# Kernel tuning notes

Hardware: AMD Instinct MI355X
Metric: run time of the kernel (lower is better)

The kernel has to match this reference:

```python
import jax, jax.numpy as jnp
import numpy as np

ALPHA = 1.0
BETA = 0.5

B, N, E = 4096, 4096, 16384


def setup_inputs() -> dict:
    key = jax.random.key(0)
    k1, k2, k3, k4, k5 = jax.random.split(key, 5)
    outputs = jax.random.normal(k1, (B, N), dtype=jnp.float32)
    targets = jax.random.uniform(k2, (B, N), dtype=jnp.float32)
    # per-node level weight (equivalent to node_levels dict -> level_weights lookup)
    level_w = jax.random.uniform(k3, (N,), dtype=jnp.float32)
    edge_src = jax.random.randint(k4, (E,), 0, N, dtype=jnp.int32)  # parent i
    edge_dst = jax.random.randint(k5, (E,), 0, N, dtype=jnp.int32)  # child  j
    return {"outputs": outputs, "targets": targets, "level_w": level_w,
            "edge_src": edge_src, "edge_dst": edge_dst}


def reference(outputs, targets, level_w, edge_src, edge_dst):
    # BCEWithLogits, reduction='none': softplus(x) - x*t (numerically stable)
    bce = jax.nn.softplus(outputs) - outputs * targets          # [B, N]
    weighted_bce = bce * level_w[None, :]                        # [B, N]

    probs = jax.nn.sigmoid(outputs)                              # [B, N]
    # for each edge (i=parent, j=child): consistency[:, j] += relu(p[:, j] - p[:, i])
    diff = jax.nn.relu(probs[:, edge_dst] - probs[:, edge_src])  # [B, E]
    consistency = jnp.zeros_like(probs).at[:, edge_dst].add(diff)  # [B, N]

    return ALPHA * weighted_bce.mean() + BETA * consistency.mean()
```

## Files before the change

### kernel.cpp

```cpp
#include <hip/hip_runtime.h>
#include <math.h>


#define ALPHA_C 1.0f
#define BETA_C  0.5f

constexpr int B = 4096;
constexpr int N = 4096;
constexpr int E = 16384;
constexpr int THREADS = 1024;
constexpr int R = 4;
constexpr int GRID = 256;
constexpr int GPB = (B / R) / GRID;
constexpr int EJ = E / 4 / THREADS;

typedef _Float16 h4 __attribute__((ext_vector_type(4)));

__global__ __launch_bounds__(64) void init_out_kernel(float* out) {
    if (threadIdx.x == 0) out[0] = 0.0f;
}

__device__ __forceinline__ void fast_sig_sp(float x, float& p, float& sp) {
    float q = __expf(-fabsf(x));
    float d = 1.0f + q;
    float r = __builtin_amdgcn_rcpf(d);
    p  = (x >= 0.0f) ? r : q * r;
    sp = fmaxf(x, 0.0f) + __logf(d);
}

__global__ __launch_bounds__(THREADS, 4) void hier_loss_kernel(
    const float* __restrict__ outputs,
    const float* __restrict__ targets,
    const float* __restrict__ level_w,
    const int*   __restrict__ edge_src,
    const int*   __restrict__ edge_dst,
    float*       __restrict__ out)
{
    __shared__ h4 P[2][N];

    const int tid = threadIdx.x;
    const int g0  = blockIdx.x * GPB;

    const float4* out4 = (const float4*)outputs;
    const float4* tgt4 = (const float4*)targets;
    const float4* lw4  = (const float4*)level_w;
    const int4*   es4  = (const int4*)edge_src;
    const int4*   ed4  = (const int4*)edge_dst;

    const float4 w = lw4[tid];
    const float wv[4] = {w.x, w.y, w.z, w.w};

    int4 se[EJ], de[EJ];
#pragma unroll
    for (int j = 0; j < EJ; ++j) {
        se[j] = es4[tid + j * THREADS];
        de[j] = ed4[tid + j * THREADS];
    }

    float s1 = 0.0f, s2 = 0.0f;
    float4 xs[R], ts[R];

#pragma unroll
    for (int r = 0; r < R; ++r) {
        const size_t row = (size_t)((g0 + 0) * R + r) * (N / 4) + tid;
        xs[r] = out4[row];
        ts[r] = tgt4[row];
    }
    {
        h4 tmp[4];
#pragma unroll
        for (int r = 0; r < R; ++r) {
            const float xv[4] = {xs[r].x, xs[r].y, xs[r].z, xs[r].w};
            const float tv[4] = {ts[r].x, ts[r].y, ts[r].z, ts[r].w};
#pragma unroll
            for (int k = 0; k < 4; ++k) {
                float p, sp;
                fast_sig_sp(xv[k], p, sp);
                s1 = fmaf(wv[k], sp - xv[k] * tv[k], s1);
                tmp[k][r] = (_Float16)p;
            }
        }
#pragma unroll
        for (int k = 0; k < 4; ++k) P[0][4 * tid + k] = tmp[k];
    }
    __syncthreads();

#pragma unroll
    for (int kg = 0; kg < GPB; ++kg) {
        if (kg + 1 < GPB) {
#pragma unroll
            for (int r = 0; r < R; ++r) {
                const size_t row = (size_t)((g0 + kg + 1) * R + r) * (N / 4) + tid;
                xs[r] = out4[row];
                ts[r] = tgt4[row];
            }
        }

        const h4* Pc = P[kg & 1];
        h4 acc0 = {0, 0, 0, 0};
        h4 acc1 = {0, 0, 0, 0};
        const h4 zero = {0, 0, 0, 0};
#pragma unroll
        for (int j = 0; j < EJ; ++j) {
            const int4 s = se[j];
            const int4 d = de[j];
            h4 a0 = Pc[s.x], c0 = Pc[d.x];
            h4 a1 = Pc[s.y], c1 = Pc[d.y];
            h4 a2 = Pc[s.z], c2 = Pc[d.z];
            h4 a3 = Pc[s.w], c3 = Pc[d.w];
            acc0 += __builtin_elementwise_max(c0 - a0, zero);
            acc1 += __builtin_elementwise_max(c1 - a1, zero);
            acc0 += __builtin_elementwise_max(c2 - a2, zero);
            acc1 += __builtin_elementwise_max(c3 - a3, zero);
        }
#pragma unroll
        for (int l = 0; l < 4; ++l) s2 += (float)acc0[l] + (float)acc1[l];

        if (kg + 1 < GPB) {
            h4 tmp[4];
#pragma unroll
            for (int r = 0; r < R; ++r) {
                const float xv[4] = {xs[r].x, xs[r].y, xs[r].z, xs[r].w};
                const float tv[4] = {ts[r].x, ts[r].y, ts[r].z, ts[r].w};
#pragma unroll
                for (int k = 0; k < 4; ++k) {
                    float p, sp;
                    fast_sig_sp(xv[k], p, sp);
                    s1 = fmaf(wv[k], sp - xv[k] * tv[k], s1);
                    tmp[k][r] = (_Float16)p;
                }
            }
#pragma unroll
            for (int k = 0; k < 4; ++k) P[(kg + 1) & 1][4 * tid + k] = tmp[k];
        }
        __syncthreads();
    }

#pragma unroll
    for (int off = 32; off > 0; off >>= 1) {
        s1 += __shfl_down(s1, off, 64);
        s2 += __shfl_down(s2, off, 64);
    }
    float* red = (float*)P;
    const int wave = tid >> 6;
    const int lane = tid & 63;
    if (lane == 0) { red[wave] = s1; red[16 + wave] = s2; }
    __syncthreads();
    if (tid == 0) {
        float a = 0.0f, c = 0.0f;
#pragma unroll
        for (int v = 0; v < 16; ++v) { a += red[v]; c += red[16 + v]; }
        const float inv = 1.0f / ((float)B * (float)N);
        atomicAdd(out, (ALPHA_C * a + BETA_C * c) * inv);
    }
}

extern "C" void kernel_launch(void* const* d_in, const int* in_sizes, int n_in,
                              void* d_out, int out_size, void* d_ws, size_t ws_size,
                              hipStream_t stream) {
    const float* outputs = (const float*)d_in[0];
    const float* targets = (const float*)d_in[1];
    const float* level_w = (const float*)d_in[2];
    const int*   edge_src = (const int*)d_in[3];
    const int*   edge_dst = (const int*)d_in[4];
    float* out = (float*)d_out;

    init_out_kernel<<<1, 64, 0, stream>>>(out);
    hier_loss_kernel<<<GRID, THREADS, 0, stream>>>(outputs, targets, level_w,
                                                   edge_src, edge_dst, out);
}
```

Measured before the change: 154.6 us.

## Split block into producer and consumer warps with swizzled shared memory layout

Warp-specializes the block: half the threads load rows and compute BCE and fp16 probabilities into a double-buffered shared tile, while the other half hold the edge lists and gather from the previous buffer. The two roles overlap across pipeline steps that are separated by block barriers. It also XOR-swizzles the shared-memory layout of probability groups to reduce bank conflicts on writes and gathers. In exchange, each role has only half the threads for its work, and edges per consumer thread and columns per producer thread both double, which raises register pressure.

```diff
diff --git a/kernel.cpp b/kernel.cpp
--- a/kernel.cpp
+++ b/kernel.cpp
@@ -9,10 +9,14 @@
 constexpr int N = 4096;
 constexpr int E = 16384;
 constexpr int THREADS = 1024;
+constexpr int GRID = 256;
 constexpr int R = 4;
-constexpr int GRID = 256;
-constexpr int GPB = (B / R) / GRID;
-constexpr int EJ = E / 4 / THREADS;
+constexpr int ROWS_PB = B / GRID;
+constexpr int GPB = ROWS_PB / R;
+constexpr int PTHREADS = 512;
+constexpr int CTHREADS = THREADS - PTHREADS;
+constexpr int CPT = (N / 4) / PTHREADS;
+constexpr int EPC = E / 4 / CTHREADS;
 
 typedef _Float16 h4 __attribute__((ext_vector_type(4)));
 
@@ -28,6 +32,8 @@
     sp = fmaxf(x, 0.0f) + __logf(d);
 }
 
+__device__ __forceinline__ int swz(int n) { return n ^ ((n >> 4) & 3); }
+
 __global__ __launch_bounds__(THREADS, 4) void hier_loss_kernel(
     const float* __restrict__ outputs,
     const float* __restrict__ targets,
@@ -38,102 +44,95 @@
 {
     __shared__ h4 P[2][N];
 
-    const int tid = threadIdx.x;
-    const int g0  = blockIdx.x * GPB;
-
-    const float4* out4 = (const float4*)outputs;
-    const float4* tgt4 = (const float4*)targets;
-    const float4* lw4  = (const float4*)level_w;
-    const int4*   es4  = (const int4*)edge_src;
-    const int4*   ed4  = (const int4*)edge_dst;
-
-    const float4 w = lw4[tid];
-    const float wv[4] = {w.x, w.y, w.z, w.w};
-
-    int4 se[EJ], de[EJ];
-#pragma unroll
-    for (int j = 0; j < EJ; ++j) {
-        se[j] = es4[tid + j * THREADS];
-        de[j] = ed4[tid + j * THREADS];
-    }
+    const int tid  = threadIdx.x;
+    const int row0 = blockIdx.x * ROWS_PB;
 
     float s1 = 0.0f, s2 = 0.0f;
-    float4 xs[R], ts[R];
 
+    if (tid < PTHREADS) {
+        const float4* out4 = (const float4*)outputs;
+        const float4* tgt4 = (const float4*)targets;
+        const float4* lw4  = (const float4*)level_w;
+
+        float wv[CPT][4];
 #pragma unroll
-    for (int r = 0; r < R; ++r) {
-        const size_t row = (size_t)((g0 + 0) * R + r) * (N / 4) + tid;
-        xs[r] = out4[row];
-        ts[r] = tgt4[row];
-    }
-    {
-        h4 tmp[4];
+        for (int c = 0; c < CPT; ++c) {
+            const float4 w = lw4[tid + c * PTHREADS];
+            wv[c][0] = w.x; wv[c][1] = w.y; wv[c][2] = w.z; wv[c][3] = w.w;
+        }
+        const int kx = (tid >> 2) & 3;
+
+        for (int step = 0; step < GPB + 1; ++step) {
+            if (step < GPB) {
+                float4 xs[CPT][R], ts[CPT][R];
 #pragma unroll
-        for (int r = 0; r < R; ++r) {
-            const float xv[4] = {xs[r].x, xs[r].y, xs[r].z, xs[r].w};
-            const float tv[4] = {ts[r].x, ts[r].y, ts[r].z, ts[r].w};
+                for (int c = 0; c < CPT; ++c)
 #pragma unroll
-            for (int k = 0; k < 4; ++k) {
-                float p, sp;
-                fast_sig_sp(xv[k], p, sp);
-                s1 = fmaf(wv[k], sp - xv[k] * tv[k], s1);
-                tmp[k][r] = (_Float16)p;
+                for (int r = 0; r < R; ++r) {
+                    const size_t idx =
+                        (size_t)(row0 + step * R + r) * (N / 4) + tid + c * PTHREADS;
+                    xs[c][r] = out4[idx];
+                    ts[c][r] = tgt4[idx];
+                }
+                h4* Pb = P[step & 1];
+#pragma unroll
+                for (int c = 0; c < CPT; ++c) {
+                    h4 tmp[4];
+#pragma unroll
+                    for (int r = 0; r < R; ++r) {
+                        const float xv[4] = {xs[c][r].x, xs[c][r].y, xs[c][r].z, xs[c][r].w};
+                        const float tv[4] = {ts[c][r].x, ts[c][r].y, ts[c][r].z, ts[c][r].w};
+#pragma unroll
+                        for (int k = 0; k < 4; ++k) {
+                            float p, sp;
+                            fast_sig_sp(xv[k], p, sp);
+                            s1 = fmaf(wv[c][k], sp - xv[k] * tv[k], s1);
+                            tmp[k][r] = (_Float16)p;
+                        }
+                    }
+                    const int base = 4 * (tid + c * PTHREADS);
+#pragma unroll
+                    for (int k = 0; k < 4; ++k) Pb[base + (k ^ kx)] = tmp[k];
+                }
             }
+            __syncthreads();
         }
+    } else {
+        const int ct = tid - PTHREADS;
+        const int4* es4 = (const int4*)edge_src;
+        const int4* ed4 = (const int4*)edge_dst;
+
+        int4 se[EPC], de[EPC];
 #pragma unroll
-        for (int k = 0; k < 4; ++k) P[0][4 * tid + k] = tmp[k];
-    }
-    __syncthreads();
-
-#pragma unroll
-    for (int kg = 0; kg < GPB; ++kg) {
-        if (kg + 1 < GPB) {
-#pragma unroll
-            for (int r = 0; r < R; ++r) {
-                const size_t row = (size_t)((g0 + kg + 1) * R + r) * (N / 4) + tid;
-                xs[r] = out4[row];
-                ts[r] = tgt4[row];
-            }
+        for (int j = 0; j < EPC; ++j) {
+            se[j] = es4[ct + j * CTHREADS];
+            de[j] = ed4[ct + j * CTHREADS];
         }
 
-        const h4* Pc = P[kg & 1];
-        h4 acc0 = {0, 0, 0, 0};
-        h4 acc1 = {0, 0, 0, 0};
-        const h4 zero = {0, 0, 0, 0};
+        for (int step = 0; step < GPB + 1; ++step) {
+            if (step >= 1) {
+                const h4* Pc = P[(step - 1) & 1];
+                h4 acc0 = {0, 0, 0, 0};
+                h4 acc1 = {0, 0, 0, 0};
+                const h4 zero = {0, 0, 0, 0};
 #pragma unroll
-        for (int j = 0; j < EJ; ++j) {
-            const int4 s = se[j];
-            const int4 d = de[j];
-            h4 a0 = Pc[s.x], c0 = Pc[d.x];
-            h4 a1 = Pc[s.y], c1 = Pc[d.y];
-            h4 a2 = Pc[s.z], c2 = Pc[d.z];
-            h4 a3 = Pc[s.w], c3 = Pc[d.w];
-            acc0 += __builtin_elementwise_max(c0 - a0, zero);
-            acc1 += __builtin_elementwise_max(c1 - a1, zero);
-            acc0 += __builtin_elementwise_max(c2 - a2, zero);
-            acc1 += __builtin_elementwise_max(c3 - a3, zero);
+                for (int j = 0; j < EPC; ++j) {
+                    const int4 s = se[j];
+                    const int4 d = de[j];
+                    h4 a0 = Pc[swz(s.x)], c0 = Pc[swz(d.x)];
+                    h4 a1 = Pc[swz(s.y)], c1 = Pc[swz(d.y)];
+                    h4 a2 = Pc[swz(s.z)], c2 = Pc[swz(d.z)];
+                    h4 a3 = Pc[swz(s.w)], c3 = Pc[swz(d.w)];
+                    acc0 += __builtin_elementwise_max(c0 - a0, zero);
+                    acc1 += __builtin_elementwise_max(c1 - a1, zero);
+                    acc0 += __builtin_elementwise_max(c2 - a2, zero);
+                    acc1 += __builtin_elementwise_max(c3 - a3, zero);
+                }
+#pragma unroll
+                for (int l = 0; l < 4; ++l) s2 += (float)acc0[l] + (float)acc1[l];
+            }
+            __syncthreads();
         }
-#pragma unroll
-        for (int l = 0; l < 4; ++l) s2 += (float)acc0[l] + (float)acc1[l];
-
-        if (kg + 1 < GPB) {
-            h4 tmp[4];
-#pragma unroll
-            for (int r = 0; r < R; ++r) {
-                const float xv[4] = {xs[r].x, xs[r].y, xs[r].z, xs[r].w};
-                const float tv[4] = {ts[r].x, ts[r].y, ts[r].z, ts[r].w};
-#pragma unroll
-                for (int k = 0; k < 4; ++k) {
-                    float p, sp;
-                    fast_sig_sp(xv[k], p, sp);
-                    s1 = fmaf(wv[k], sp - xv[k] * tv[k], s1);
-                    tmp[k][r] = (_Float16)p;
-                }
-            }
-#pragma unroll
-            for (int k = 0; k < 4; ++k) P[(kg + 1) & 1][4 * tid + k] = tmp[k];
-        }
-        __syncthreads();
     }
 
 #pragma unroll
```

After: 162.9 us. +5.4%, slower.
